# Optimization experiments

Measured on AMD Instinct MI355X. Metric: run time of the kernel, lower is better.

The kernel has to match this reference:

```python
import jax, jax.numpy as jnp
import numpy as np

D = 1024
H = 16
HD = D // H
DFF = 4 * D
LN_EPS = 1e-5

def layernorm(x, gamma, beta):
    mu = jnp.mean(x, axis=-1, keepdims=True)
    var = jnp.mean(jnp.square(x - mu), axis=-1, keepdims=True)
    return (x - mu) * jax.lax.rsqrt(var + LN_EPS) * gamma + beta

def setup_inputs() -> dict:
    key = jax.random.key(0)
    ks = jax.random.split(key, 10)
    B, Nq, Nk = 2, 2048, 2048
    s = 0.02
    return {
        "q_x": jax.random.normal(ks[0], (B, Nq, D), jnp.float32),
        "kv_x": jax.random.normal(ks[1], (B, Nk, D), jnp.float32),
        "Wq": jax.random.normal(ks[2], (D, D), jnp.float32) * s,
        "Wkv": jax.random.normal(ks[3], (2 * D, D), jnp.float32) * s,
        "Wo": jax.random.normal(ks[4], (D, D), jnp.float32) * s,
        "bo": jnp.zeros((D,), jnp.float32),
        "ln_q_g": jnp.ones((D,), jnp.float32),
        "ln_q_b": jnp.zeros((D,), jnp.float32),
        "ln_kv_g": jnp.ones((D,), jnp.float32),
        "ln_kv_b": jnp.zeros((D,), jnp.float32),
        "W1": jax.random.normal(ks[5], (DFF, D), jnp.float32) * s,
        "b1": jnp.zeros((DFF,), jnp.float32),
        "W2": jax.random.normal(ks[6], (D, DFF), jnp.float32) * s,
        "b2": jnp.zeros((D,), jnp.float32),
    }

def reference(q_x, kv_x, Wq, Wkv, Wo, bo, ln_q_g, ln_q_b, ln_kv_g, ln_kv_b, W1, b1, W2, b2):
    B, Nq, _ = q_x.shape
    Nk = kv_x.shape[1]
    scale = HD ** -0.5
    # norm + projections
    q = layernorm(q_x, ln_q_g, ln_q_b) @ Wq.T                    # [B,Nq,D]
    kv = layernorm(kv_x, ln_kv_g, ln_kv_b) @ Wkv.T               # [B,Nk,2D]
    q = q.reshape(B, Nq, H, HD).transpose(0, 2, 1, 3)            # [B,H,Nq,hd]
    kv = kv.reshape(B, Nk, 2, H, HD).transpose(2, 0, 3, 1, 4)    # [2,B,H,Nk,hd]
    k, v = kv[0], kv[1]
    attn = jnp.einsum('bhqd,bhkd->bhqk', q, k) * scale           # [B,H,Nq,Nk]
    attn = jax.nn.softmax(attn, axis=-1)
    out = jnp.einsum('bhqk,bhkd->bhqd', attn, v)
    out = out.transpose(0, 2, 1, 3).reshape(B, Nq, D)
    x = q_x + out @ Wo.T + bo
    h = jax.nn.silu(x @ W1.T + b1)
    x = x + h @ W2.T + b2
    return x
```

## Files before the change

kernel.cpp:

```cpp
#include <hip/hip_runtime.h>

using u16   = unsigned short;
using f32x4 = __attribute__((ext_vector_type(4))) float;
using s16x8 = __attribute__((ext_vector_type(8))) short;
using u32x2 = __attribute__((ext_vector_type(2))) unsigned int;
using u32x4 = __attribute__((ext_vector_type(4))) unsigned int;

#define LOG2E 1.44269504088896f

static __device__ __forceinline__ u16 f2bf(float f) {
  union { float f; unsigned u; } a; a.f = f;
  unsigned r = a.u + 0x7fffu + ((a.u >> 16) & 1u);
  return (u16)(r >> 16);
}
static __device__ __forceinline__ unsigned cvtpk(float lo, float hi) {
  unsigned r;
  asm("v_cvt_pk_bf16_f32 %0, %1, %2" : "=v"(r) : "v"(lo), "v"(hi));
  return r;
}

static __device__ __forceinline__ void gload16(const void* g, void* l) {
  __builtin_amdgcn_global_load_lds(
      (__attribute__((address_space(1))) unsigned int*)g,
      (__attribute__((address_space(3))) unsigned int*)l, 16, 0, 0);
}

__global__ __launch_bounds__(256) void prep_k(
    const float* __restrict__ Wq, const float* __restrict__ Wkv,
    const float* __restrict__ Wo, const float* __restrict__ W1,
    const float* __restrict__ W2,
    u16* __restrict__ wq_b, u16* __restrict__ wkv_b, u16* __restrict__ wo_b,
    u16* __restrict__ w1_b, u16* __restrict__ w2_b,
    const float* __restrict__ xq, const float* __restrict__ xk,
    const float* __restrict__ gq, const float* __restrict__ bq,
    const float* __restrict__ gk, const float* __restrict__ bk,
    u16* __restrict__ oq, u16* __restrict__ ok)
{
  const int blk = blockIdx.x, t = threadIdx.x;
  if (blk < 12288) {
    const int i = blk * 256 + t;
    const float* src; u16* dst; int off; float sc = 1.0f;
    if      (i <  262144) { src = Wq;  dst = wq_b;  off = i; sc = 0.125f * LOG2E; }
    else if (i <  786432) { src = Wkv; dst = wkv_b; off = i -  262144; }
    else if (i < 1048576) { src = Wo;  dst = wo_b;  off = i -  786432; }
    else if (i < 2097152) { src = W1;  dst = w1_b;  off = i - 1048576; }
    else                  { src = W2;  dst = w2_b;  off = i - 2097152; }
    const float4 v = ((const float4*)src)[off];
    ushort4 o;
    o.x = f2bf(v.x * sc); o.y = f2bf(v.y * sc); o.z = f2bf(v.z * sc); o.w = f2bf(v.w * sc);
    ((ushort4*)dst)[off] = o;
    return;
  }
  int row = blk - 12288;
  const float* x; const float* gam; const float* bet; u16* out;
  if (row < 4096) { x = xq; gam = gq; bet = bq; out = oq; }
  else { row -= 4096; x = xk; gam = gk; bet = bk; out = ok; }
  const float4 v = ((const float4*)(x + (size_t)row * 1024))[t];
  float s  = v.x + v.y + v.z + v.w;
  float ss = v.x*v.x + v.y*v.y + v.z*v.z + v.w*v.w;
  #pragma unroll
  for (int m = 1; m < 64; m <<= 1) { s += __shfl_xor(s, m); ss += __shfl_xor(ss, m); }
  __shared__ float red[8];
  const int w = t >> 6;
  if ((t & 63) == 0) { red[w] = s; red[4 + w] = ss; }
  __syncthreads();
  s  = red[0] + red[1] + red[2] + red[3];
  ss = red[4] + red[5] + red[6] + red[7];
  const float mu   = s * (1.0f / 1024.0f);
  const float rstd = rsqrtf(ss * (1.0f / 1024.0f) - mu * mu + 1e-5f);
  const float4 gv = ((const float4*)gam)[t];
  const float4 bv = ((const float4*)bet)[t];
  ushort4 o;
  o.x = f2bf((v.x - mu) * rstd * gv.x + bv.x);
  o.y = f2bf((v.y - mu) * rstd * gv.y + bv.y);
  o.z = f2bf((v.z - mu) * rstd * gv.z + bv.z);
  o.w = f2bf((v.w - mu) * rstd * gv.w + bv.w);
  ((ushort4*)(out + (size_t)row * 1024))[t] = o;
}

template<int BIAS, int RES, int SILU, int OF32, int OBF>
static __device__ __forceinline__ void gemm_body(
    const u16* __restrict__ A, const u16* __restrict__ B,
    u16* __restrict__ Cb, float* __restrict__ Cf,
    const float* __restrict__ bias, const float* __restrict__ resid,
    int N, int K, int bid, u16* smem)
{
  const int tid = threadIdx.x;
  const int w = tid >> 6, l = tid & 63;
  const int g = l >> 4, q = l & 15;
  const int ntn = N >> 7;
  const int bm = bid / ntn, bn = bid - bm * ntn;
  const int wr = w >> 1, wc = w & 1;
  const int sw = (q & 7) << 4;
  f32x4 acc[2][4] = {};

  const size_t abase = (size_t)(bm * 128) * K;
  const size_t bbase = (size_t)(bn * 128) * K;

  auto stage = [&](int buf, int k0) {
    u16* as = smem + buf * 8192;
    u16* bs = smem + 16384 + buf * 8192;
    #pragma unroll
    for (int r = 0; r < 2; ++r) {
      const int c = (r << 9) + tid;
      const int row = c >> 3, part = c & 7;
      const int sp = part ^ (row & 7);
      gload16(A + abase + (size_t)row * K + k0 + sp * 8,
              as + (size_t)((r << 9) + (w << 6)) * 8);
      gload16(B + bbase + (size_t)row * K + k0 + sp * 8,
              bs + (size_t)((r << 9) + (w << 6)) * 8);
    }
  };

  const int NT = K >> 6;
  stage(0, 0);
  asm volatile("s_waitcnt vmcnt(0)" ::: "memory");
  __syncthreads();
  int cur = 0;
  for (int t = 0; t < NT; ++t) {
    if (t + 1 < NT) stage(cur ^ 1, (t + 1) << 6);
    const char* as = (const char*)(smem + cur * 8192);
    const char* bs = (const char*)(smem + 16384 + cur * 8192);
    #pragma unroll
    for (int ks = 0; ks < 2; ++ks) {
      s16x8 af[2], bfr[4];
      #pragma unroll
      for (int m = 0; m < 2; ++m)
        af[m] = *(const s16x8*)(as + (size_t)(wr * 32 + m * 16 + q) * 128 +
                                ((ks * 64 + g * 16) ^ sw));
      #pragma unroll
      for (int n = 0; n < 4; ++n)
        bfr[n] = *(const s16x8*)(bs + (size_t)(wc * 64 + n * 16 + q) * 128 +
                                 ((ks * 64 + g * 16) ^ sw));
      #pragma unroll
      for (int m = 0; m < 2; ++m)
        #pragma unroll
        for (int n = 0; n < 4; ++n)
          acc[m][n] = __builtin_amdgcn_mfma_f32_16x16x32_bf16(af[m], bfr[n], acc[m][n], 0, 0, 0);
    }
    asm volatile("s_waitcnt vmcnt(0)" ::: "memory");
    __syncthreads();
    cur ^= 1;
  }

  #pragma unroll
  for (int m = 0; m < 2; ++m) {
    const int row0 = bm * 128 + wr * 32 + m * 16 + g * 4;
    #pragma unroll
    for (int n = 0; n < 4; ++n) {
      const int col = bn * 128 + wc * 64 + n * 16 + q;
      float bv = 0.0f;
      if (BIAS) bv = bias[col];
      #pragma unroll
      for (int r = 0; r < 4; ++r) {
        const size_t idx = (size_t)(row0 + r) * N + col;
        float v = acc[m][n][r] + bv;
        if (RES)  v += resid[idx];
        if (SILU) v = v / (1.0f + __expf(-v));
        if (OF32) Cf[idx] = v;
        if (OBF)  Cb[idx] = f2bf(v);
      }
    }
  }
}

template<int BIAS, int RES, int SILU, int OF32, int OBF>
__global__ __launch_bounds__(512, 4) void gemm_k(
    const u16* __restrict__ A, const u16* __restrict__ B,
    u16* __restrict__ Cb, float* __restrict__ Cf,
    const float* __restrict__ bias, const float* __restrict__ resid,
    int N, int K)
{
  __shared__ u16 smem[32768];
  gemm_body<BIAS, RES, SILU, OF32, OBF>(A, B, Cb, Cf, bias, resid, N, K, blockIdx.x, smem);
}

__global__ __launch_bounds__(512, 4) void gemm_qkv_k(
    const u16* __restrict__ lnq, const u16* __restrict__ wq, u16* __restrict__ qp,
    const u16* __restrict__ lnk, const u16* __restrict__ wkv, u16* __restrict__ kvp)
{
  __shared__ u16 smem[32768];
  if (blockIdx.x < 256)
    gemm_body<0,0,0,0,1>(lnq, wq, qp, nullptr, nullptr, nullptr, 1024, 1024, blockIdx.x, smem);
  else
    gemm_body<0,0,0,0,1>(lnk, wkv, kvp, nullptr, nullptr, nullptr, 2048, 1024, blockIdx.x - 256, smem);
}

template<int BIAS, int RES, int SILU, int OF32, int OBF>
__global__ __launch_bounds__(512, 2) void gemm256_k(
    const u16* __restrict__ A, const u16* __restrict__ B,
    u16* __restrict__ Cb, float* __restrict__ Cf,
    const float* __restrict__ bias, const float* __restrict__ resid,
    int N, int K)
{
  __shared__ u16 smem[65536];
  char* smem_c = (char*)smem;
  const int tid = threadIdx.x;
  const int w = tid >> 6, l = tid & 63;
  const int g = l >> 4, q = l & 15;
  const int wm = w >> 2, wn = w & 3;
  const int ntn = N >> 8;
  const int nwg = gridDim.x;
  const int bid = (blockIdx.x % 8) * (nwg / 8) + blockIdx.x / 8;
  const int bm = bid / ntn, bn = bid - bm * ntn;

  const size_t abase = (size_t)(bm * 256) * K;
  const size_t bbase = (size_t)(bn * 256) * K;

  f32x4 acc[8][4] = {};

  auto stage4 = [&](int buf, int kt, int halfsel) {
    #pragma unroll
    for (int rr = 0; rr < 4; ++rr) {
      const int r = halfsel * 4 + rr;
      const int isB   = (r >> 1) & 1;
      const int khalf = r >> 2;
      const int sub   = r & 1;
      const int row   = sub * 128 + (tid >> 2);
      const int slot  = (tid & 3) ^ ((row >> 1) & 3);
      const u16* src = (isB ? B + bbase : A + abase)
                     + (size_t)row * K + kt * 64 + khalf * 32 + slot * 8;
      char* dst = smem_c + buf * 65536 + isB * 32768 + khalf * 16384
                + sub * 8192 + w * 1024;
      gload16(src, dst);
    }
  };

  const int NT = K >> 6;
  stage4(0, 0, 0); stage4(0, 0, 1);
  int cur = 0;
  for (int kt = 0; kt < NT; ++kt) {
    const bool pre = (kt + 1 < NT);
    if (pre) stage4(cur ^ 1, kt + 1, 0);
    if (pre) asm volatile("s_waitcnt vmcnt(4)" ::: "memory");
    else     asm volatile("s_waitcnt vmcnt(0)" ::: "memory");
    __builtin_amdgcn_s_barrier();
    asm volatile("" ::: "memory");
    const char* Ab0 = smem_c + cur * 65536;
    const char* Bb0 = Ab0 + 32768;
    const int so = (g ^ ((q >> 1) & 3)) * 16;
    #pragma unroll
    for (int ks = 0; ks < 2; ++ks) {
      const char* Ab = Ab0 + ks * 16384;
      const char* Bb = Bb0 + ks * 16384;
      s16x8 af[8], bfr[4];
      #pragma unroll
      for (int m = 0; m < 8; ++m)
        af[m] = *(const s16x8*)(Ab + (wm * 128 + m * 16 + q) * 64 + so);
      #pragma unroll
      for (int n = 0; n < 4; ++n)
        bfr[n] = *(const s16x8*)(Bb + (wn * 64 + n * 16 + q) * 64 + so);
      if (ks == 0 && pre) stage4(cur ^ 1, kt + 1, 1);
      asm volatile("s_waitcnt lgkmcnt(0)" ::: "memory");
      __builtin_amdgcn_sched_barrier(0);
      __builtin_amdgcn_s_setprio(1);
      #pragma unroll
      for (int m = 0; m < 8; ++m)
        #pragma unroll
        for (int n = 0; n < 4; ++n)
          acc[m][n] = __builtin_amdgcn_mfma_f32_16x16x32_bf16(af[m], bfr[n], acc[m][n], 0, 0, 0);
      __builtin_amdgcn_s_setprio(0);
    }
    asm volatile("" ::: "memory");
    __builtin_amdgcn_s_barrier();
    asm volatile("" ::: "memory");
    cur ^= 1;
  }

  #pragma unroll
  for (int m = 0; m < 8; ++m) {
    const int row0 = bm * 256 + wm * 128 + m * 16 + g * 4;
    #pragma unroll
    for (int n = 0; n < 4; ++n) {
      const int col = bn * 256 + wn * 64 + n * 16 + q;
      float bv = 0.0f;
      if (BIAS) bv = bias[col];
      #pragma unroll
      for (int r = 0; r < 4; ++r) {
        const size_t idx = (size_t)(row0 + r) * N + col;
        float v = acc[m][n][r] + bv;
        if (RES)  v += resid[idx];
        if (SILU) v = v / (1.0f + __expf(-v));
        if (OF32) Cf[idx] = v;
        if (OBF)  Cb[idx] = f2bf(v);
      }
    }
  }
}

__global__ __launch_bounds__(256, 4) void attn_k(
    const u16* __restrict__ Q, const u16* __restrict__ KV, u16* __restrict__ O)
{
  __shared__ u16 Ks[2][64 * 64];
  __shared__ u16 Vs[2][64 * 64];
  const int tid = threadIdx.x;
  const int w = tid >> 6, l = tid & 63;
  const int g = l >> 4, q = l & 15;
  const int bh = blockIdx.x >> 5, qt = blockIdx.x & 31;
  const int b = bh >> 4, h = bh & 15;

  const size_t qrow = (size_t)(b * 2048 + qt * 64 + w * 16 + q);
  s16x8 qf[2];
  qf[0] = *(const s16x8*)&Q[qrow * 1024 + h * 64 + g * 8];
  qf[1] = *(const s16x8*)&Q[qrow * 1024 + h * 64 + 32 + g * 8];

  f32x4 oacc[4] = {};
  float mrow = -1e30f, lrow = 0.0f;

  const u16* kvb = KV + (size_t)b * 2048 * 2048;
  const unsigned vs_base =
      (unsigned)(unsigned long long)(__attribute__((address_space(3))) u16*)Vs;

  auto stage = [&](int buf, int kv0) {
    #pragma unroll
    for (int r = 0; r < 2; ++r) {
      const int c = (r << 8) + tid;
      const int krow = c >> 3, slot = c & 7;
      gload16(kvb + (size_t)(kv0 + krow) * 2048 + h * 64 + ((slot ^ (krow & 7)) << 3),
              &Ks[buf][(size_t)((r << 8) + (w << 6)) * 8]);
      const int vkv = ((c >> 3) & 15) * 4 + ((c >> 1) & 3);
      const int vd0 = ((c >> 7) & 3) * 16 + (c & 1) * 8;
      gload16(kvb + (size_t)(kv0 + vkv) * 2048 + 1024 + h * 64 + vd0,
              &Vs[buf][(size_t)((r << 8) + (w << 6)) * 8]);
    }
  };

  stage(0, 0);
  asm volatile("s_waitcnt vmcnt(0)" ::: "memory");
  __syncthreads();
  int cur = 0;

  for (int kt = 0; kt < 32; ++kt) {
    if (kt + 1 < 32) stage(cur ^ 1, (kt + 1) * 64);

    const char* ksb = (const char*)Ks[cur];
    f32x4 sacc[4] = {};
    __builtin_amdgcn_s_setprio(1);
    #pragma unroll
    for (int s = 0; s < 2; ++s)
      #pragma unroll
      for (int nf = 0; nf < 4; ++nf) {
        const int krw = nf * 16 + q;
        const s16x8 kf = *(const s16x8*)(ksb + krw * 128 +
                              ((s * 64 + g * 16) ^ ((krw & 7) << 4)));
        sacc[nf] = __builtin_amdgcn_mfma_f32_16x16x32_bf16(kf, qf[s], sacc[nf], 0, 0, 0);
      }
    __builtin_amdgcn_s_setprio(0);

    float mx = sacc[0][0];
    #pragma unroll
    for (int nf = 0; nf < 4; ++nf)
      #pragma unroll
      for (int r = 0; r < 4; ++r) mx = fmaxf(mx, sacc[nf][r]);
    mx = fmaxf(mx, __shfl_xor(mx, 16));
    mx = fmaxf(mx, __shfl_xor(mx, 32));
    if (__any(mx > mrow + 8.0f)) {
      const float mnew = fmaxf(mrow, mx);
      const float al = __builtin_amdgcn_exp2f(mrow - mnew);
      lrow *= al;
      float ar[4];
      #pragma unroll
      for (int r = 0; r < 4; ++r) ar[r] = __shfl(al, g * 4 + r);
      #pragma unroll
      for (int nf = 0; nf < 4; ++nf)
        #pragma unroll
        for (int r = 0; r < 4; ++r) oacc[nf][r] *= ar[r];
      mrow = mnew;
    }
    float rs = 0.0f;
    #pragma unroll
    for (int nf = 0; nf < 4; ++nf)
      #pragma unroll
      for (int r = 0; r < 4; ++r) {
        const float e = __builtin_amdgcn_exp2f(sacc[nf][r] - mrow);
        sacc[nf][r] = e; rs += e;
      }
    rs += __shfl_xor(rs, 16);
    rs += __shfl_xor(rs, 32);
    lrow += rs;

    union { u32x4 u; s16x8 s8; } au[2];
    #pragma unroll
    for (int s = 0; s < 2; ++s) {
      au[s].u[0] = cvtpk(sacc[2*s  ][0], sacc[2*s  ][1]);
      au[s].u[1] = cvtpk(sacc[2*s  ][2], sacc[2*s  ][3]);
      au[s].u[2] = cvtpk(sacc[2*s+1][0], sacc[2*s+1][1]);
      au[s].u[3] = cvtpk(sacc[2*s+1][2], sacc[2*s+1][3]);
    }

    const unsigned a0 = vs_base + (unsigned)(cur << 13) + (unsigned)(g * 128 + 2 * q);
    u32x2 v0,v1,v2,v3,v4,v5,v6,v7,v8,v9,v10,v11,v12,v13,v14,v15;
    asm volatile(
        "ds_read_b64_tr_b16 %0,  %16\n\t"
        "ds_read_b64_tr_b16 %1,  %16 offset:512\n\t"
        "ds_read_b64_tr_b16 %2,  %16 offset:2048\n\t"
        "ds_read_b64_tr_b16 %3,  %16 offset:2560\n\t"
        "ds_read_b64_tr_b16 %4,  %16 offset:4096\n\t"
        "ds_read_b64_tr_b16 %5,  %16 offset:4608\n\t"
        "ds_read_b64_tr_b16 %6,  %16 offset:6144\n\t"
        "ds_read_b64_tr_b16 %7,  %16 offset:6656\n\t"
        "ds_read_b64_tr_b16 %8,  %16 offset:1024\n\t"
        "ds_read_b64_tr_b16 %9,  %16 offset:1536\n\t"
        "ds_read_b64_tr_b16 %10, %16 offset:3072\n\t"
        "ds_read_b64_tr_b16 %11, %16 offset:3584\n\t"
        "ds_read_b64_tr_b16 %12, %16 offset:5120\n\t"
        "ds_read_b64_tr_b16 %13, %16 offset:5632\n\t"
        "ds_read_b64_tr_b16 %14, %16 offset:7168\n\t"
        "ds_read_b64_tr_b16 %15, %16 offset:7680\n\t"
        "s_waitcnt lgkmcnt(0)"
        : "=&v"(v0), "=&v"(v1), "=&v"(v2),  "=&v"(v3),
          "=&v"(v4), "=&v"(v5), "=&v"(v6),  "=&v"(v7),
          "=&v"(v8), "=&v"(v9), "=&v"(v10), "=&v"(v11),
          "=&v"(v12),"=&v"(v13),"=&v"(v14), "=&v"(v15)
        : "v"(a0) : "memory");
    __builtin_amdgcn_sched_barrier(0);

    __builtin_amdgcn_s_setprio(1);
    {
      union { u32x4 u; s16x8 s8; } bu;
      bu.u[0]=v0[0];  bu.u[1]=v0[1];  bu.u[2]=v1[0];  bu.u[3]=v1[1];
      oacc[0] = __builtin_amdgcn_mfma_f32_16x16x32_bf16(au[0].s8, bu.s8, oacc[0], 0, 0, 0);
      bu.u[0]=v2[0];  bu.u[1]=v2[1];  bu.u[2]=v3[0];  bu.u[3]=v3[1];
      oacc[1] = __builtin_amdgcn_mfma_f32_16x16x32_bf16(au[0].s8, bu.s8, oacc[1], 0, 0, 0);
      bu.u[0]=v4[0];  bu.u[1]=v4[1];  bu.u[2]=v5[0];  bu.u[3]=v5[1];
      oacc[2] = __builtin_amdgcn_mfma_f32_16x16x32_bf16(au[0].s8, bu.s8, oacc[2], 0, 0, 0);
      bu.u[0]=v6[0];  bu.u[1]=v6[1];  bu.u[2]=v7[0];  bu.u[3]=v7[1];
      oacc[3] = __builtin_amdgcn_mfma_f32_16x16x32_bf16(au[0].s8, bu.s8, oacc[3], 0, 0, 0);
      bu.u[0]=v8[0];  bu.u[1]=v8[1];  bu.u[2]=v9[0];  bu.u[3]=v9[1];
      oacc[0] = __builtin_amdgcn_mfma_f32_16x16x32_bf16(au[1].s8, bu.s8, oacc[0], 0, 0, 0);
      bu.u[0]=v10[0]; bu.u[1]=v10[1]; bu.u[2]=v11[0]; bu.u[3]=v11[1];
      oacc[1] = __builtin_amdgcn_mfma_f32_16x16x32_bf16(au[1].s8, bu.s8, oacc[1], 0, 0, 0);
      bu.u[0]=v12[0]; bu.u[1]=v12[1]; bu.u[2]=v13[0]; bu.u[3]=v13[1];
      oacc[2] = __builtin_amdgcn_mfma_f32_16x16x32_bf16(au[1].s8, bu.s8, oacc[2], 0, 0, 0);
      bu.u[0]=v14[0]; bu.u[1]=v14[1]; bu.u[2]=v15[0]; bu.u[3]=v15[1];
      oacc[3] = __builtin_amdgcn_mfma_f32_16x16x32_bf16(au[1].s8, bu.s8, oacc[3], 0, 0, 0);
    }
    __builtin_amdgcn_s_setprio(0);

    asm volatile("s_waitcnt vmcnt(0)" ::: "memory");
    __syncthreads();
    cur ^= 1;
  }

  float lr[4];
  #pragma unroll
  for (int r = 0; r < 4; ++r) lr[r] = __shfl(lrow, g * 4 + r);
  const size_t ob = (size_t)(b * 2048 + qt * 64 + w * 16) * 1024 + h * 64;
  #pragma unroll
  for (int r = 0; r < 4; ++r) {
    const float inv = 1.0f / lr[r];
    #pragma unroll
    for (int nf = 0; nf < 4; ++nf)
      O[ob + (size_t)(g * 4 + r) * 1024 + nf * 16 + q] = f2bf(oacc[nf][r] * inv);
  }
}

extern "C" void kernel_launch(void* const* d_in, const int* in_sizes, int n_in,
                              void* d_out, int out_size, void* d_ws, size_t ws_size,
                              hipStream_t stream)
{
  const float* q_x  = (const float*)d_in[0];
  const float* kv_x = (const float*)d_in[1];
  const float* Wq   = (const float*)d_in[2];
  const float* Wkv  = (const float*)d_in[3];
  const float* Wo   = (const float*)d_in[4];
  const float* bo   = (const float*)d_in[5];
  const float* lnqg = (const float*)d_in[6];
  const float* lnqb = (const float*)d_in[7];
  const float* lnkg = (const float*)d_in[8];
  const float* lnkb = (const float*)d_in[9];
  const float* W1   = (const float*)d_in[10];
  const float* b1   = (const float*)d_in[11];
  const float* W2   = (const float*)d_in[12];
  const float* b2   = (const float*)d_in[13];
  float* out = (float*)d_out;

  char* ws = (char*)d_ws;
  const size_t MB = 1024 * 1024;
  u16*   wq_b  = (u16*)  (ws +  0 * MB);
  u16*   wkv_b = (u16*)  (ws +  2 * MB);
  u16*   wo_b  = (u16*)  (ws +  6 * MB);
  u16*   w1_b  = (u16*)  (ws +  8 * MB);
  u16*   w2_b  = (u16*)  (ws + 16 * MB);
  u16*   lnq   = (u16*)  (ws + 24 * MB);
  u16*   lnk   = (u16*)  (ws + 32 * MB);
  u16*   qp    = (u16*)  (ws + 40 * MB);
  u16*   kvp   = (u16*)  (ws + 48 * MB);
  u16*   ao    = (u16*)  (ws + 64 * MB);
  float* xf    = (float*)(ws + 72 * MB);
  u16*   xb    = (u16*)  (ws + 88 * MB);
  u16*   hb    = (u16*)  (ws + 96 * MB);

  prep_k<<<dim3(20480), dim3(256), 0, stream>>>(
      Wq, Wkv, Wo, W1, W2, wq_b, wkv_b, wo_b, w1_b, w2_b,
      q_x, kv_x, lnqg, lnqb, lnkg, lnkb, lnq, lnk);

  gemm_qkv_k<<<dim3(768), dim3(512), 0, stream>>>(lnq, wq_b, qp, lnk, wkv_b, kvp);
  attn_k<<<dim3(1024), dim3(256), 0, stream>>>(qp, kvp, ao);
  gemm_k<1,1,0,1,1><<<dim3(256),  dim3(512), 0, stream>>>(
      ao, wo_b, xb, xf, bo, q_x, 1024, 1024);
  gemm256_k<1,0,1,0,1><<<dim3(256), dim3(512), 0, stream>>>(
      xb, w1_b, hb, nullptr, b1, nullptr, 4096, 1024);
  gemm_k<1,1,0,1,0><<<dim3(256),  dim3(512), 0, stream>>>(
      hb, w2_b, nullptr, out, b2, xf, 1024, 4096);
}
```

Before: 227.4 us.

## Split GEMM K-tile prefetch into four phases and remap attention blocks across XCDs

The GEMM main loop now issues next-tile global-to-LDS loads in four smaller parts, each interleaved with a half-width MFMA batch. Barriers move to the start of each k-substep, with vmcnt waits tuned per phase, so memory latency overlaps compute more evenly and the trailing barrier goes away. Separately, attention blocks are remapped so that consecutive block IDs, which land on different XCDs, spread over (batch, head) groups. This should improve per-XCD L2 reuse of K/V. In exchange the pipeline adds more barriers and more waitcnt points, and it relies on exact load counts for correctness.

```diff
diff --git a/kernel.cpp b/kernel.cpp
--- a/kernel.cpp
+++ b/kernel.cpp
@@ -209,15 +209,12 @@
 
   f32x4 acc[8][4] = {};
 
-  auto stage4 = [&](int buf, int kt, int halfsel) {
-    #pragma unroll
-    for (int rr = 0; rr < 4; ++rr) {
-      const int r = halfsel * 4 + rr;
-      const int isB   = (r >> 1) & 1;
-      const int khalf = r >> 2;
-      const int sub   = r & 1;
-      const int row   = sub * 128 + (tid >> 2);
-      const int slot  = (tid & 3) ^ ((row >> 1) & 3);
+  auto stage2 = [&](int buf, int kt, int part) {
+    const int isB = part & 1, khalf = part >> 1;
+    #pragma unroll
+    for (int sub = 0; sub < 2; ++sub) {
+      const int row  = sub * 128 + (tid >> 2);
+      const int slot = (tid & 3) ^ ((row >> 1) & 3);
       const u16* src = (isB ? B + bbase : A + abase)
                      + (size_t)row * K + kt * 64 + khalf * 32 + slot * 8;
       char* dst = smem_c + buf * 65536 + isB * 32768 + khalf * 16384
@@ -227,43 +224,53 @@
   };
 
   const int NT = K >> 6;
-  stage4(0, 0, 0); stage4(0, 0, 1);
+  stage2(0, 0, 0); stage2(0, 0, 1); stage2(0, 0, 2); stage2(0, 0, 3);
   int cur = 0;
-  for (int kt = 0; kt < NT; ++kt) {
-    const bool pre = (kt + 1 < NT);
-    if (pre) stage4(cur ^ 1, kt + 1, 0);
-    if (pre) asm volatile("s_waitcnt vmcnt(4)" ::: "memory");
-    else     asm volatile("s_waitcnt vmcnt(0)" ::: "memory");
-    __builtin_amdgcn_s_barrier();
-    asm volatile("" ::: "memory");
-    const char* Ab0 = smem_c + cur * 65536;
-    const char* Bb0 = Ab0 + 32768;
-    const int so = (g ^ ((q >> 1) & 3)) * 16;
+  const int so = (g ^ ((q >> 1) & 3)) * 16;
+  for (int t = 0; t < NT; ++t) {
+    const bool pre = (t + 1 < NT);
+    const char* base = smem_c + cur * 65536;
     #pragma unroll
     for (int ks = 0; ks < 2; ++ks) {
-      const char* Ab = Ab0 + ks * 16384;
-      const char* Bb = Bb0 + ks * 16384;
-      s16x8 af[8], bfr[4];
+      if (ks == 0 || pre) asm volatile("s_waitcnt vmcnt(4)" ::: "memory");
+      else                asm volatile("s_waitcnt vmcnt(0)" ::: "memory");
+      asm volatile("" ::: "memory");
+      __builtin_amdgcn_s_barrier();
+      asm volatile("" ::: "memory");
+      const char* Ab = base + ks * 16384;
+      const char* Bb = base + 32768 + ks * 16384;
+      s16x8 af[8], bf0[2];
       #pragma unroll
       for (int m = 0; m < 8; ++m)
         af[m] = *(const s16x8*)(Ab + (wm * 128 + m * 16 + q) * 64 + so);
       #pragma unroll
-      for (int n = 0; n < 4; ++n)
-        bfr[n] = *(const s16x8*)(Bb + (wn * 64 + n * 16 + q) * 64 + so);
-      if (ks == 0 && pre) stage4(cur ^ 1, kt + 1, 1);
+      for (int n = 0; n < 2; ++n)
+        bf0[n] = *(const s16x8*)(Bb + (wn * 64 + n * 16 + q) * 64 + so);
+      if (pre) stage2(cur ^ 1, t + 1, ks * 2);
       asm volatile("s_waitcnt lgkmcnt(0)" ::: "memory");
       __builtin_amdgcn_sched_barrier(0);
       __builtin_amdgcn_s_setprio(1);
       #pragma unroll
-      for (int m = 0; m < 8; ++m)
-        #pragma unroll
-        for (int n = 0; n < 4; ++n)
-          acc[m][n] = __builtin_amdgcn_mfma_f32_16x16x32_bf16(af[m], bfr[n], acc[m][n], 0, 0, 0);
+      for (int m = 0; m < 8; ++m) {
+        acc[m][0] = __builtin_amdgcn_mfma_f32_16x16x32_bf16(af[m], bf0[0], acc[m][0], 0, 0, 0);
+        acc[m][1] = __builtin_amdgcn_mfma_f32_16x16x32_bf16(af[m], bf0[1], acc[m][1], 0, 0, 0);
+      }
       __builtin_amdgcn_s_setprio(0);
-    }
-    asm volatile("" ::: "memory");
-    __builtin_amdgcn_s_barrier();
-    asm volatile("" ::: "memory");
+      s16x8 bf1[2];
+      #pragma unroll
+      for (int n = 0; n < 2; ++n)
+        bf1[n] = *(const s16x8*)(Bb + (wn * 64 + (2 + n) * 16 + q) * 64 + so);
+      if (pre) stage2(cur ^ 1, t + 1, ks * 2 + 1);
+      asm volatile("s_waitcnt lgkmcnt(0)" ::: "memory");
+      __builtin_amdgcn_sched_barrier(0);
+      __builtin_amdgcn_s_setprio(1);
+      #pragma unroll
+      for (int m = 0; m < 8; ++m) {
+        acc[m][2] = __builtin_amdgcn_mfma_f32_16x16x32_bf16(af[m], bf1[0], acc[m][2], 0, 0, 0);
+        acc[m][3] = __builtin_amdgcn_mfma_f32_16x16x32_bf16(af[m], bf1[1], acc[m][3], 0, 0, 0);
+      }
+      __builtin_amdgcn_s_setprio(0);
+    }
     cur ^= 1;
   }
 
@@ -296,7 +303,9 @@
   const int tid = threadIdx.x;
   const int w = tid >> 6, l = tid & 63;
   const int g = l >> 4, q = l & 15;
-  const int bh = blockIdx.x >> 5, qt = blockIdx.x & 31;
+  const int idx = blockIdx.x >> 3;
+  const int bh = (blockIdx.x & 7) * 4 + (idx >> 5);
+  const int qt = idx & 31;
   const int b = bh >> 4, h = bh & 15;
 
   const size_t qrow = (size_t)(b * 2048 + qt * 64 + w * 16 + q);
```

New measurement: 221.5 us. 1.03x faster.
